# Kernel tuning notes

Measured on AMD Instinct MI355X. Metric: run time of the kernel, lower is better.

Reference implementation:

```python
import jax, jax.numpy as jnp
import numpy as np

K = 10          # hardcoded in module (self.K = 10)
H = 26          # neighbors per query point in this run
PAD_H = 28      # layer_ind2neighbor[layer_ind=0]
KP_EXTENT = 1.2 # linear-influence extent


def setup_inputs() -> dict:
    key = jax.random.key(0)
    ks = jax.random.split(key, 6)
    N, Ns, Cin, Cout = 65536, 65536, 64, 128
    q_pts = jax.random.normal(ks[0], (N, 3), jnp.float32)
    s_pts = jax.random.normal(ks[1], (Ns, 3), jnp.float32)
    neighb_inds = jax.random.randint(ks[2], (N, H), 0, Ns)
    x = jax.random.normal(ks[3], (Ns, Cin), jnp.float32)
    # kernel_points_generator: Linear(PAD_H*3 -> K*3)
    gen_W = jax.random.normal(ks[4], (K * 3, PAD_H * 3), jnp.float32) * (1.0 / np.sqrt(PAD_H * 3))
    gen_b = jnp.zeros((K * 3,), jnp.float32)
    # KPConv weights: [K, in, out] (kaiming_uniform in torch; scaled normal here)
    weights = jax.random.normal(ks[5], (K, Cin, Cout), jnp.float32) * (1.0 / np.sqrt(Cin))
    return {"q_pts": q_pts, "s_pts": s_pts, "x": x,
            "gen_W": gen_W, "gen_b": gen_b, "weights": weights,
            "neighb_inds": neighb_inds}


def _kpconv(q_pts, s_pts, x, gen_W, gen_b, weights, neighb_inds):
    N = q_pts.shape[0]
    # shadow support point far away (index Ns)
    s_pad = jnp.concatenate([s_pts, jnp.full((1, 3), 1e6, s_pts.dtype)], axis=0)
    neighbors = s_pad[neighb_inds] - q_pts[:, None, :]                          # [N,H,3]
    # generative kernel points: pad neighbor list with -1 up to PAD_H, run linear
    padded = jnp.concatenate(
        [neighbors, jnp.full((N, PAD_H - H, 3), -1.0, neighbors.dtype)], axis=1)
    kp = (padded.reshape(N, -1) @ gen_W.T + gen_b).reshape(N, 1, K, 3)          # [N,1,K,3]
    diff = neighbors[:, :, None, :] - kp                                        # [N,H,K,3]
    sq_d = jnp.sum(diff * diff, axis=3)                                         # [N,H,K]
    # KP_influence == 'linear'
    all_w = jnp.maximum(1.0 - jnp.sqrt(sq_d) / KP_EXTENT, 0.0)
    all_w = jnp.swapaxes(all_w, 1, 2)                                           # [N,K,H]
    # shadow feature row (zeros) at index Ns
    x_pad = jnp.concatenate([x, jnp.zeros((1, x.shape[1]), x.dtype)], axis=0)
    neighb_x = x_pad[neighb_inds]                                               # [N,H,Cin]
    weighted = jnp.einsum('nkh,nhi->nki', all_w, neighb_x)                      # [N,K,Cin]
    return jnp.einsum('nki,kio->no', weighted, weights)                         # [N,Cout]


def reference(q_pts, s_pts, x, gen_W, gen_b, weights, neighb_inds):
    return _kpconv(q_pts, s_pts, x, gen_W, gen_b, weights, neighb_inds)
```

## Files before the change

kernel.cpp:

```cpp
#include <hip/hip_runtime.h>
#include <stdint.h>

#define N_Q   65536
#define N_S   65536
#define NB_H  26
#define PAD_H 28
#define KP    10
#define CIN   64
#define COUT  128
#define MT    16
#define BM    64

typedef unsigned short u16x4  __attribute__((ext_vector_type(4)));
typedef unsigned short u16x8  __attribute__((ext_vector_type(8)));
typedef float          f32x4  __attribute__((ext_vector_type(4)));
typedef __bf16         bf16x8 __attribute__((ext_vector_type(8)));

#define CVT_BLOCKS 2049
#define PACK_BLOCKS 40

static __device__ __forceinline__ unsigned short f2bf(float f) {
  unsigned int u = __float_as_uint(f);
  u += 0x7fffu + ((u >> 16) & 1u);
  return (unsigned short)(u >> 16);
}
static __device__ __forceinline__ float bf2f(unsigned short h) {
  return __uint_as_float(((unsigned int)h) << 16);
}

__global__ void prep_kernel(const float* __restrict__ x,
                            const float* __restrict__ w,
                            unsigned short* __restrict__ xb,
                            unsigned short* __restrict__ bp) {
  if (blockIdx.x < CVT_BLOCKS) {
    long t = (long)blockIdx.x * blockDim.x + threadIdx.x;
    long off = t * 8;
    if (off >= (long)(N_S + 1) * CIN) return;
    u16x8 o;
    if (off < (long)N_S * CIN) {
      f32x4 a = *(const f32x4*)(x + off);
      f32x4 b = *(const f32x4*)(x + off + 4);
      o[0] = f2bf(a[0]); o[1] = f2bf(a[1]); o[2] = f2bf(a[2]); o[3] = f2bf(a[3]);
      o[4] = f2bf(b[0]); o[5] = f2bf(b[1]); o[6] = f2bf(b[2]); o[7] = f2bf(b[3]);
    } else {
      o = (u16x8)0;
    }
    *(u16x8*)(xb + off) = o;
  } else {
    int t = (blockIdx.x - CVT_BLOCKS) * blockDim.x + threadIdx.x;
    if (t >= 8 * 20 * 64) return;
    int lane = t & 63;
    int frag = t >> 6;
    int ks = frag % 20;
    int ct = frag / 20;
    int row0 = ks * 32 + (lane >> 4) * 8;
    int col  = ct * 16 + (lane & 15);
    u16x8 o;
    #pragma unroll
    for (int j = 0; j < 8; ++j) o[j] = f2bf(w[(row0 + j) * COUT + col]);
    *(u16x8*)(bp + (long)t * 8) = o;
  }
}

__global__ void __launch_bounds__(256, 4)
kpconv_gather(const float* __restrict__ q_pts, const float* __restrict__ s_pts,
              const float* __restrict__ gen_W, const float* __restrict__ gen_b,
              const int* __restrict__ inds, const unsigned short* __restrict__ xb,
              unsigned short* __restrict__ wg) {

  __shared__ int   sh_ind[MT][NB_H];
  __shared__ float sh_nbr[MT][NB_H][3];
  __shared__ float sh_kp[MT][KP * 3];
  __shared__ float sh_aw[MT][NB_H * KP];

  const int tid  = threadIdx.x;
  const int base = blockIdx.x * MT;

  for (int p = tid; p < MT * NB_H; p += 256) {
    int m = p / NB_H, h = p % NB_H;
    int n = base + m;
    int ind = inds[n * NB_H + h];
    sh_ind[m][h] = ind;
    float sx, sy, sz;
    if ((unsigned)ind < (unsigned)N_S) {
      sx = s_pts[ind * 3 + 0]; sy = s_pts[ind * 3 + 1]; sz = s_pts[ind * 3 + 2];
    } else {
      sx = 1e6f; sy = 1e6f; sz = 1e6f;
    }
    sh_nbr[m][h][0] = sx - q_pts[n * 3 + 0];
    sh_nbr[m][h][1] = sy - q_pts[n * 3 + 1];
    sh_nbr[m][h][2] = sz - q_pts[n * 3 + 2];
  }
  __syncthreads();

  for (int p = tid; p < MT * KP * 3; p += 256) {
    int m = p / (KP * 3), r = p % (KP * 3);
    const float* Wr = gen_W + r * (PAD_H * 3);
    float acc = gen_b[r];
    #pragma unroll
    for (int c = NB_H * 3; c < PAD_H * 3; ++c) acc -= Wr[c];
    for (int h = 0; h < NB_H; ++h) {
      acc += Wr[h * 3 + 0] * sh_nbr[m][h][0]
           + Wr[h * 3 + 1] * sh_nbr[m][h][1]
           + Wr[h * 3 + 2] * sh_nbr[m][h][2];
    }
    sh_kp[m][r] = acc;
  }
  __syncthreads();

  for (int p = tid; p < MT * KP * NB_H; p += 256) {
    int m = p / (KP * NB_H);
    int r = p - m * (KP * NB_H);
    int k = r / NB_H, h = r % NB_H;
    float dx = sh_nbr[m][h][0] - sh_kp[m][k * 3 + 0];
    float dy = sh_nbr[m][h][1] - sh_kp[m][k * 3 + 1];
    float dz = sh_nbr[m][h][2] - sh_kp[m][k * 3 + 2];
    float d  = sqrtf(dx * dx + dy * dy + dz * dz);
    sh_aw[m][h * KP + k] = fmaxf(1.0f - d * (1.0f / 1.2f), 0.0f);
  }
  __syncthreads();

  {
    const int m  = tid >> 4;
    const int i0 = (tid & 15) * 4;
    float acc[KP][4];
    #pragma unroll
    for (int k = 0; k < KP; ++k)
      #pragma unroll
      for (int j = 0; j < 4; ++j) acc[k][j] = 0.0f;

    u16x4 xr[5];
    #pragma unroll
    for (int h = 0; h < 5; ++h)
      xr[h] = *(const u16x4*)(xb + (long)sh_ind[m][h] * CIN + i0);

    #pragma unroll
    for (int h = 0; h < NB_H; ++h) {
      u16x4 xc = xr[h % 5];
      if (h + 5 < NB_H)
        xr[h % 5] = *(const u16x4*)(xb + (long)sh_ind[m][h + 5] * CIN + i0);
      float xf0 = bf2f(xc[0]), xf1 = bf2f(xc[1]);
      float xf2 = bf2f(xc[2]), xf3 = bf2f(xc[3]);
      const float* wrow = &sh_aw[m][h * KP];
      #pragma unroll
      for (int k = 0; k < KP; ++k) {
        float w = wrow[k];
        acc[k][0] = fmaf(w, xf0, acc[k][0]);
        acc[k][1] = fmaf(w, xf1, acc[k][1]);
        acc[k][2] = fmaf(w, xf2, acc[k][2]);
        acc[k][3] = fmaf(w, xf3, acc[k][3]);
      }
    }
    #pragma unroll
    for (int k = 0; k < KP; ++k) {
      u16x4 o;
      #pragma unroll
      for (int j = 0; j < 4; ++j) o[j] = f2bf(acc[k][j]);
      *(u16x4*)(wg + (long)(base + m) * (KP * CIN) + k * CIN + i0) = o;
    }
  }
}

__global__ void __launch_bounds__(256, 4)
kpconv_gemm(const unsigned short* __restrict__ wg,
            const unsigned short* __restrict__ bp,
            float* __restrict__ out) {

  __shared__ unsigned short sA[2][BM][72];

  const int tid  = threadIdx.x;
  const int wave = tid >> 6;
  const int lane = tid & 63;
  const long row0 = (long)blockIdx.x * BM;

  const int srow = tid >> 3;
  const int scb  = tid & 7;

  {
    u16x8 a = *(const u16x8*)(wg + (row0 + srow) * 640 + scb * 8);
    u16x8 b = *(const u16x8*)(wg + (row0 + srow + 32) * 640 + scb * 8);
    *(u16x8*)&sA[0][srow][scb * 8] = a;
    *(u16x8*)&sA[0][srow + 32][scb * 8] = b;
  }

  f32x4 acc[4][2];
  #pragma unroll
  for (int rt = 0; rt < 4; ++rt)
    #pragma unroll
    for (int c = 0; c < 2; ++c) acc[rt][c] = (f32x4){0.f, 0.f, 0.f, 0.f};

  const int ct0  = wave * 2, ct1 = ct0 + 1;
  const int arow = lane & 15;
  const int aq   = lane >> 4;
  int cur = 0;

  for (int kc = 0; kc < 10; ++kc) {
    __syncthreads();
    u16x8 p0, p1;
    if (kc < 9) {
      p0 = *(const u16x8*)(wg + (row0 + srow) * 640 + (kc + 1) * 64 + scb * 8);
      p1 = *(const u16x8*)(wg + (row0 + srow + 32) * 640 + (kc + 1) * 64 + scb * 8);
    }
    #pragma unroll
    for (int ks2 = 0; ks2 < 2; ++ks2) {
      int ks = kc * 2 + ks2;
      u16x8 b0u = *(const u16x8*)(bp + (long)((ct0 * 20 + ks) * 64 + lane) * 8);
      u16x8 b1u = *(const u16x8*)(bp + (long)((ct1 * 20 + ks) * 64 + lane) * 8);
      bf16x8 b0 = __builtin_bit_cast(bf16x8, b0u);
      bf16x8 b1 = __builtin_bit_cast(bf16x8, b1u);
      #pragma unroll
      for (int rt = 0; rt < 4; ++rt) {
        u16x8 au = *(const u16x8*)&sA[cur][rt * 16 + arow][ks2 * 32 + aq * 8];
        bf16x8 a = __builtin_bit_cast(bf16x8, au);
        acc[rt][0] = __builtin_amdgcn_mfma_f32_16x16x32_bf16(a, b0, acc[rt][0], 0, 0, 0);
        acc[rt][1] = __builtin_amdgcn_mfma_f32_16x16x32_bf16(a, b1, acc[rt][1], 0, 0, 0);
      }
    }
    if (kc < 9) {
      *(u16x8*)&sA[1 - cur][srow][scb * 8] = p0;
      *(u16x8*)&sA[1 - cur][srow + 32][scb * 8] = p1;
      cur ^= 1;
    }
  }

  const int col   = lane & 15;
  const int rbase = aq * 4;
  #pragma unroll
  for (int rt = 0; rt < 4; ++rt)
    #pragma unroll
    for (int r = 0; r < 4; ++r) {
      long row = row0 + rt * 16 + rbase + r;
      out[row * COUT + ct0 * 16 + col] = acc[rt][0][r];
      out[row * COUT + ct1 * 16 + col] = acc[rt][1][r];
    }
}

extern "C" void kernel_launch(void* const* d_in, const int* in_sizes, int n_in,
                              void* d_out, int out_size, void* d_ws, size_t ws_size,
                              hipStream_t stream) {
  const float* q_pts = (const float*)d_in[0];
  const float* s_pts = (const float*)d_in[1];
  const float* x     = (const float*)d_in[2];
  const float* gen_W = (const float*)d_in[3];
  const float* gen_b = (const float*)d_in[4];
  const float* wts   = (const float*)d_in[5];
  const int*   inds  = (const int*)d_in[6];
  float* out = (float*)d_out;

  unsigned short* xb = (unsigned short*)d_ws;
  unsigned short* bp = xb + (size_t)(N_S + 1) * CIN;
  unsigned short* wg = bp + (size_t)81920;

  prep_kernel<<<CVT_BLOCKS + PACK_BLOCKS, 256, 0, stream>>>(x, wts, xb, bp);
  kpconv_gather<<<N_Q / MT, 256, 0, stream>>>(q_pts, s_pts, gen_W, gen_b,
                                              inds, xb, wg);
  kpconv_gemm<<<N_Q / BM, 256, 0, stream>>>(wg, bp, out);
}
```

Baseline: 189.9 us.

## Switch to fp16 with packed dot2 accumulation and halve gather tile

Intermediate data moves from bf16 to fp16. The gather inner loop now uses packed fp16 weights with v_dot2 instructions over neighbor pairs, and the GEMM uses f16 MFMA. The gather tile drops to 8 points per block with higher occupancy bounds, the kernel-point linear layer is vectorized over a padded neighbor row, and nontemporal loads and stores are added for the intermediate and output. This is meant to cut ALU work and improve latency hiding in the gather. In exchange fp16 has less range than bf16, and the weights round toward zero on conversion.

```diff
diff --git a/kernel.cpp b/kernel.cpp
--- a/kernel.cpp
+++ b/kernel.cpp
@@ -8,29 +8,39 @@
 #define KP    10
 #define CIN   64
 #define COUT  128
-#define MT    16
+#define MT    8
 #define BM    64
 
 typedef unsigned short u16x4  __attribute__((ext_vector_type(4)));
 typedef unsigned short u16x8  __attribute__((ext_vector_type(8)));
 typedef float          f32x4  __attribute__((ext_vector_type(4)));
-typedef __bf16         bf16x8 __attribute__((ext_vector_type(8)));
+typedef _Float16       f16x8  __attribute__((ext_vector_type(8)));
+typedef _Float16       f16x2  __attribute__((ext_vector_type(2)));
 
 #define CVT_BLOCKS 2049
 #define PACK_BLOCKS 40
 
-static __device__ __forceinline__ unsigned short f2bf(float f) {
-  unsigned int u = __float_as_uint(f);
-  u += 0x7fffu + ((u >> 16) & 1u);
-  return (unsigned short)(u >> 16);
-}
-static __device__ __forceinline__ float bf2f(unsigned short h) {
-  return __uint_as_float(((unsigned int)h) << 16);
+static __device__ __forceinline__ unsigned short f2h(float f) {
+  return __builtin_bit_cast(unsigned short, (_Float16)f);
+}
+
+static __device__ __forceinline__ unsigned int pkrtz_u32(float a, float b) {
+  return __builtin_bit_cast(unsigned int, __builtin_amdgcn_cvt_pkrtz(a, b));
+}
+
+static __device__ __forceinline__ float fdot2u(unsigned int a, unsigned int b, float c) {
+#if __has_builtin(__builtin_amdgcn_fdot2)
+  return __builtin_amdgcn_fdot2(__builtin_bit_cast(f16x2, a),
+                                __builtin_bit_cast(f16x2, b), c, false);
+#else
+  f16x2 ha = __builtin_bit_cast(f16x2, a), hb = __builtin_bit_cast(f16x2, b);
+  return c + (float)ha[0] * (float)hb[0] + (float)ha[1] * (float)hb[1];
+#endif
 }
 
 __global__ void prep_kernel(const float* __restrict__ x,
                             const float* __restrict__ w,
-                            unsigned short* __restrict__ xb,
+                            unsigned short* __restrict__ xh,
                             unsigned short* __restrict__ bp) {
   if (blockIdx.x < CVT_BLOCKS) {
     long t = (long)blockIdx.x * blockDim.x + threadIdx.x;
@@ -40,12 +50,12 @@
     if (off < (long)N_S * CIN) {
       f32x4 a = *(const f32x4*)(x + off);
       f32x4 b = *(const f32x4*)(x + off + 4);
-      o[0] = f2bf(a[0]); o[1] = f2bf(a[1]); o[2] = f2bf(a[2]); o[3] = f2bf(a[3]);
-      o[4] = f2bf(b[0]); o[5] = f2bf(b[1]); o[6] = f2bf(b[2]); o[7] = f2bf(b[3]);
+      o[0] = f2h(a[0]); o[1] = f2h(a[1]); o[2] = f2h(a[2]); o[3] = f2h(a[3]);
+      o[4] = f2h(b[0]); o[5] = f2h(b[1]); o[6] = f2h(b[2]); o[7] = f2h(b[3]);
     } else {
       o = (u16x8)0;
     }
-    *(u16x8*)(xb + off) = o;
+    *(u16x8*)(xh + off) = o;
   } else {
     int t = (blockIdx.x - CVT_BLOCKS) * blockDim.x + threadIdx.x;
     if (t >= 8 * 20 * 64) return;
@@ -57,27 +67,27 @@
     int col  = ct * 16 + (lane & 15);
     u16x8 o;
     #pragma unroll
-    for (int j = 0; j < 8; ++j) o[j] = f2bf(w[(row0 + j) * COUT + col]);
+    for (int j = 0; j < 8; ++j) o[j] = f2h(w[(row0 + j) * COUT + col]);
     *(u16x8*)(bp + (long)t * 8) = o;
   }
 }
 
-__global__ void __launch_bounds__(256, 4)
+__global__ void __launch_bounds__(256, 6)
 kpconv_gather(const float* __restrict__ q_pts, const float* __restrict__ s_pts,
               const float* __restrict__ gen_W, const float* __restrict__ gen_b,
-              const int* __restrict__ inds, const unsigned short* __restrict__ xb,
+              const int* __restrict__ inds, const unsigned short* __restrict__ xh,
               unsigned short* __restrict__ wg) {
 
-  __shared__ int   sh_ind[MT][NB_H];
-  __shared__ float sh_nbr[MT][NB_H][3];
-  __shared__ float sh_kp[MT][KP * 3];
-  __shared__ float sh_aw[MT][NB_H * KP];
+  __shared__ int          sh_ind[MT][NB_H];
+  __shared__ float        sh_nbr[MT][80];
+  __shared__ float        sh_kp[MT][KP * 3];
+  __shared__ unsigned int sh_aw[MT][13][12];
 
   const int tid  = threadIdx.x;
   const int base = blockIdx.x * MT;
 
-  for (int p = tid; p < MT * NB_H; p += 256) {
-    int m = p / NB_H, h = p % NB_H;
+  if (tid < MT * NB_H) {
+    int m = tid / NB_H, h = tid % NB_H;
     int n = base + m;
     int ind = inds[n * NB_H + h];
     sh_ind[m][h] = ind;
@@ -87,76 +97,80 @@
     } else {
       sx = 1e6f; sy = 1e6f; sz = 1e6f;
     }
-    sh_nbr[m][h][0] = sx - q_pts[n * 3 + 0];
-    sh_nbr[m][h][1] = sy - q_pts[n * 3 + 1];
-    sh_nbr[m][h][2] = sz - q_pts[n * 3 + 2];
-  }
+    sh_nbr[m][h * 3 + 0] = sx - q_pts[n * 3 + 0];
+    sh_nbr[m][h * 3 + 1] = sy - q_pts[n * 3 + 1];
+    sh_nbr[m][h * 3 + 2] = sz - q_pts[n * 3 + 2];
+  }
+  if (tid < MT * 2) sh_nbr[tid >> 1][78 + (tid & 1)] = -1.0f;
   __syncthreads();
 
-  for (int p = tid; p < MT * KP * 3; p += 256) {
-    int m = p / (KP * 3), r = p % (KP * 3);
+  if (tid < MT * KP * 3) {
+    int m = tid / 30, r = tid % 30;
     const float* Wr = gen_W + r * (PAD_H * 3);
-    float acc = gen_b[r];
-    #pragma unroll
-    for (int c = NB_H * 3; c < PAD_H * 3; ++c) acc -= Wr[c];
-    for (int h = 0; h < NB_H; ++h) {
-      acc += Wr[h * 3 + 0] * sh_nbr[m][h][0]
-           + Wr[h * 3 + 1] * sh_nbr[m][h][1]
-           + Wr[h * 3 + 2] * sh_nbr[m][h][2];
-    }
-    sh_kp[m][r] = acc;
+    const f32x4* W4 = (const f32x4*)Wr;
+    const f32x4* N4 = (const f32x4*)&sh_nbr[m][0];
+    f32x4 accv = {0.f, 0.f, 0.f, 0.f};
+    #pragma unroll
+    for (int j = 0; j < 20; ++j) accv += W4[j] * N4[j];
+    sh_kp[m][r] = gen_b[r] - (Wr[80] + Wr[81] + Wr[82] + Wr[83])
+                + accv[0] + accv[1] + accv[2] + accv[3];
   }
   __syncthreads();
 
-  for (int p = tid; p < MT * KP * NB_H; p += 256) {
-    int m = p / (KP * NB_H);
-    int r = p - m * (KP * NB_H);
-    int k = r / NB_H, h = r % NB_H;
-    float dx = sh_nbr[m][h][0] - sh_kp[m][k * 3 + 0];
-    float dy = sh_nbr[m][h][1] - sh_kp[m][k * 3 + 1];
-    float dz = sh_nbr[m][h][2] - sh_kp[m][k * 3 + 2];
-    float d  = sqrtf(dx * dx + dy * dy + dz * dz);
-    sh_aw[m][h * KP + k] = fmaxf(1.0f - d * (1.0f / 1.2f), 0.0f);
+  for (int p = tid; p < MT * 13 * KP; p += 256) {
+    int k = p % KP;
+    int t = p / KP;
+    int m = t & (MT - 1);
+    int hp = t >> 3;
+    float kx = sh_kp[m][k * 3 + 0], ky = sh_kp[m][k * 3 + 1], kz = sh_kp[m][k * 3 + 2];
+    int h0 = hp * 2;
+    float dx0 = sh_nbr[m][h0 * 3 + 0] - kx;
+    float dy0 = sh_nbr[m][h0 * 3 + 1] - ky;
+    float dz0 = sh_nbr[m][h0 * 3 + 2] - kz;
+    float w0 = fmaxf(1.0f - sqrtf(dx0 * dx0 + dy0 * dy0 + dz0 * dz0) * (1.0f / 1.2f), 0.0f);
+    float dx1 = sh_nbr[m][h0 * 3 + 3] - kx;
+    float dy1 = sh_nbr[m][h0 * 3 + 4] - ky;
+    float dz1 = sh_nbr[m][h0 * 3 + 5] - kz;
+    float w1 = fmaxf(1.0f - sqrtf(dx1 * dx1 + dy1 * dy1 + dz1 * dz1) * (1.0f / 1.2f), 0.0f);
+    sh_aw[m][hp][k] = pkrtz_u32(w0, w1);
   }
   __syncthreads();
 
   {
-    const int m  = tid >> 4;
-    const int i0 = (tid & 15) * 4;
-    float acc[KP][4];
-    #pragma unroll
-    for (int k = 0; k < KP; ++k)
-      #pragma unroll
-      for (int j = 0; j < 4; ++j) acc[k][j] = 0.0f;
-
-    u16x4 xr[5];
-    #pragma unroll
-    for (int h = 0; h < 5; ++h)
-      xr[h] = *(const u16x4*)(xb + (long)sh_ind[m][h] * CIN + i0);
-
-    #pragma unroll
-    for (int h = 0; h < NB_H; ++h) {
-      u16x4 xc = xr[h % 5];
-      if (h + 5 < NB_H)
-        xr[h % 5] = *(const u16x4*)(xb + (long)sh_ind[m][h + 5] * CIN + i0);
-      float xf0 = bf2f(xc[0]), xf1 = bf2f(xc[1]);
-      float xf2 = bf2f(xc[2]), xf3 = bf2f(xc[3]);
-      const float* wrow = &sh_aw[m][h * KP];
+    const int m  = tid >> 5;
+    const int i0 = (tid & 31) * 2;
+    float acc0[KP], acc1[KP];
+    #pragma unroll
+    for (int k = 0; k < KP; ++k) { acc0[k] = 0.f; acc1[k] = 0.f; }
+
+    unsigned int xr[4];
+    #pragma unroll
+    for (int h = 0; h < 4; ++h)
+      xr[h] = *(const unsigned int*)(xh + (long)sh_ind[m][h] * CIN + i0);
+
+    #pragma unroll
+    for (int p = 0; p < 13; ++p) {
+      unsigned int r0 = xr[(2 * p) & 3];
+      unsigned int r1 = xr[(2 * p + 1) & 3];
+      if (2 * p + 4 < NB_H)
+        xr[(2 * p) & 3] = *(const unsigned int*)(xh + (long)sh_ind[m][2 * p + 4] * CIN + i0);
+      if (2 * p + 5 < NB_H)
+        xr[(2 * p + 1) & 3] = *(const unsigned int*)(xh + (long)sh_ind[m][2 * p + 5] * CIN + i0);
+      unsigned int pair0 = __builtin_amdgcn_perm(r1, r0, 0x05040100u);
+      unsigned int pair1 = __builtin_amdgcn_perm(r1, r0, 0x07060302u);
+      const unsigned int* wrow = &sh_aw[m][p][0];
       #pragma unroll
       for (int k = 0; k < KP; ++k) {
-        float w = wrow[k];
-        acc[k][0] = fmaf(w, xf0, acc[k][0]);
-        acc[k][1] = fmaf(w, xf1, acc[k][1]);
-        acc[k][2] = fmaf(w, xf2, acc[k][2]);
-        acc[k][3] = fmaf(w, xf3, acc[k][3]);
+        unsigned int w2 = wrow[k];
+        acc0[k] = fdot2u(w2, pair0, acc0[k]);
+        acc1[k] = fdot2u(w2, pair1, acc1[k]);
       }
     }
     #pragma unroll
     for (int k = 0; k < KP; ++k) {
-      u16x4 o;
-      #pragma unroll
-      for (int j = 0; j < 4; ++j) o[j] = f2bf(acc[k][j]);
-      *(u16x4*)(wg + (long)(base + m) * (KP * CIN) + k * CIN + i0) = o;
+      __builtin_nontemporal_store(
+          pkrtz_u32(acc0[k], acc1[k]),
+          (unsigned int*)(wg + (long)(base + m) * (KP * CIN) + k * CIN + i0));
     }
   }
 }
@@ -177,8 +191,8 @@
   const int scb  = tid & 7;
 
   {
-    u16x8 a = *(const u16x8*)(wg + (row0 + srow) * 640 + scb * 8);
-    u16x8 b = *(const u16x8*)(wg + (row0 + srow + 32) * 640 + scb * 8);
+    u16x8 a = __builtin_nontemporal_load((const u16x8*)(wg + (row0 + srow) * 640 + scb * 8));
+    u16x8 b = __builtin_nontemporal_load((const u16x8*)(wg + (row0 + srow + 32) * 640 + scb * 8));
     *(u16x8*)&sA[0][srow][scb * 8] = a;
     *(u16x8*)&sA[0][srow + 32][scb * 8] = b;
   }
@@ -198,22 +212,22 @@
     __syncthreads();
     u16x8 p0, p1;
     if (kc < 9) {
-      p0 = *(const u16x8*)(wg + (row0 + srow) * 640 + (kc + 1) * 64 + scb * 8);
-      p1 = *(const u16x8*)(wg + (row0 + srow + 32) * 640 + (kc + 1) * 64 + scb * 8);
+      p0 = __builtin_nontemporal_load((const u16x8*)(wg + (row0 + srow) * 640 + (kc + 1) * 64 + scb * 8));
+      p1 = __builtin_nontemporal_load((const u16x8*)(wg + (row0 + srow + 32) * 640 + (kc + 1) * 64 + scb * 8));
     }
     #pragma unroll
     for (int ks2 = 0; ks2 < 2; ++ks2) {
       int ks = kc * 2 + ks2;
       u16x8 b0u = *(const u16x8*)(bp + (long)((ct0 * 20 + ks) * 64 + lane) * 8);
       u16x8 b1u = *(const u16x8*)(bp + (long)((ct1 * 20 + ks) * 64 + lane) * 8);
-      bf16x8 b0 = __builtin_bit_cast(bf16x8, b0u);
-      bf16x8 b1 = __builtin_bit_cast(bf16x8, b1u);
+      f16x8 b0 = __builtin_bit_cast(f16x8, b0u);
+      f16x8 b1 = __builtin_bit_cast(f16x8, b1u);
       #pragma unroll
       for (int rt = 0; rt < 4; ++rt) {
         u16x8 au = *(const u16x8*)&sA[cur][rt * 16 + arow][ks2 * 32 + aq * 8];
-        bf16x8 a = __builtin_bit_cast(bf16x8, au);
-        acc[rt][0] = __builtin_amdgcn_mfma_f32_16x16x32_bf16(a, b0, acc[rt][0], 0, 0, 0);
-        acc[rt][1] = __builtin_amdgcn_mfma_f32_16x16x32_bf16(a, b1, acc[rt][1], 0, 0, 0);
+        f16x8 a = __builtin_bit_cast(f16x8, au);
+        acc[rt][0] = __builtin_amdgcn_mfma_f32_16x16x32_f16(a, b0, acc[rt][0], 0, 0, 0);
+        acc[rt][1] = __builtin_amdgcn_mfma_f32_16x16x32_f16(a, b1, acc[rt][1], 0, 0, 0);
       }
     }
     if (kc < 9) {
@@ -230,8 +244,8 @@
     #pragma unroll
     for (int r = 0; r < 4; ++r) {
       long row = row0 + rt * 16 + rbase + r;
-      out[row * COUT + ct0 * 16 + col] = acc[rt][0][r];
-      out[row * COUT + ct1 * 16 + col] = acc[rt][1][r];
+      __builtin_nontemporal_store(acc[rt][0][r], &out[row * COUT + ct0 * 16 + col]);
+      __builtin_nontemporal_store(acc[rt][1][r], &out[row * COUT + ct1 * 16 + col]);
     }
 }
 
@@ -247,12 +261,12 @@
   const int*   inds  = (const int*)d_in[6];
   float* out = (float*)d_out;
 
-  unsigned short* xb = (unsigned short*)d_ws;
-  unsigned short* bp = xb + (size_t)(N_S + 1) * CIN;
+  unsigned short* xh = (unsigned short*)d_ws;
+  unsigned short* bp = xh + (size_t)(N_S + 1) * CIN;
   unsigned short* wg = bp + (size_t)81920;
 
-  prep_kernel<<<CVT_BLOCKS + PACK_BLOCKS, 256, 0, stream>>>(x, wts, xb, bp);
+  prep_kernel<<<CVT_BLOCKS + PACK_BLOCKS, 256, 0, stream>>>(x, wts, xh, bp);
   kpconv_gather<<<N_Q / MT, 256, 0, stream>>>(q_pts, s_pts, gen_W, gen_b,
-                                              inds, xb, wg);
+                                              inds, xh, wg);
   kpconv_gemm<<<N_Q / BM, 256, 0, stream>>>(wg, bp, out);
 }
```

Measured after the change: 174.3 us. 8.2% less time.
